# Optimization experiments

Hardware: AMD Instinct MI355X
Metric: run time of the kernel (lower is better)

Reference implementation:

```python
import jax, jax.numpy as jnp
import numpy as np

WIN = 7          # window height/width
P = 10           # prompts_len
HEADS = 12
B0 = 32          # image batch (spa_prompts batch)
NW = 64          # windows per image
NW_TOK = WIN * WIN  # 49


def _relative_position_index(w):
    coords = np.stack(np.meshgrid(np.arange(w), np.arange(w), indexing='ij'))  # [2,w,w]
    flat = coords.reshape(2, -1)                        # [2, w*w]
    rel = flat[:, :, None] - flat[:, None, :]           # [2, w*w, w*w]
    rel = rel.transpose(1, 2, 0).astype(np.int64)       # [w*w, w*w, 2]
    rel[..., 0] += w - 1
    rel[..., 1] += w - 1
    rel[..., 0] *= 2 * w - 1
    return rel.sum(-1)                                  # [w*w, w*w]

REL_IDX = jnp.asarray(_relative_position_index(WIN))    # [49,49] int


def setup_inputs() -> dict:
    key = jax.random.key(0)
    ks = jax.random.split(key, 8)
    dim = 384
    return {
        'x': jax.random.normal(ks[0], (B0 * NW, NW_TOK, dim), jnp.float32),
        'spa_prompts': jax.random.normal(ks[1], (B0, P, dim), jnp.float32),
        'mask': jax.random.normal(ks[2], (NW, NW_TOK, NW_TOK), jnp.float32),
        'bias_table': jax.random.normal(ks[3], (169, HEADS), jnp.float32) * 0.02,
        'w_qkv': jax.random.normal(ks[4], (3 * dim, dim), jnp.float32) * 0.02,
        'b_qkv': jax.random.normal(ks[5], (3 * dim,), jnp.float32) * 0.02,
        'w_proj': jax.random.normal(ks[6], (dim, dim), jnp.float32) * 0.02,
        'b_proj': jax.random.normal(ks[7], (dim,), jnp.float32) * 0.02,
    }


def reference(x, spa_prompts, mask, bias_table, w_qkv, b_qkv, w_proj, b_proj):
    B_, Nw, C = x.shape
    b0 = spa_prompts.shape[0]
    nW = B_ // b0
    hd = C // HEADS
    scale = hd ** -0.5

    # broadcast prompts to every window and prepend
    prompts = jnp.broadcast_to(spa_prompts[:, None], (b0, nW, P, C)).reshape(B_, P, C)
    xc = jnp.concatenate([prompts, x], axis=1)          # [B_, N, C], N = P + Nw
    N = xc.shape[1]

    qkv = xc @ w_qkv.T + b_qkv                          # [B_, N, 3C]
    qkv = qkv.reshape(B_, N, 3, HEADS, hd).transpose(2, 0, 3, 1, 4)
    q, k, v = qkv[0], qkv[1], qkv[2]                    # [B_, H, N, hd]

    attn_weight = jnp.einsum('bhnd,bhmd->bhnm', q, k)   # unscaled, returned

    # relative position bias gathered for the window block, padded over prompt rows/cols
    rpb = bias_table[REL_IDX.reshape(-1)].reshape(NW_TOK, NW_TOK, HEADS)
    rpb = rpb.transpose(2, 0, 1)                        # [H, 49, 49]
    bias_full = jnp.pad(rpb, ((0, 0), (P, 0), (P, 0)))  # [H, N, N]

    attn = attn_weight * scale + bias_full[None]

    mask_full = jnp.pad(mask, ((0, 0), (P, 0), (P, 0)))  # [nW, N, N]
    attn = attn.reshape(b0, nW, HEADS, N, N) + mask_full[None, :, None]
    attn = jax.nn.softmax(attn.reshape(B_, HEADS, N, N), axis=-1)

    out = jnp.einsum('bhnm,bhmd->bnhd', attn, v).reshape(B_, N, C)
    out = out @ w_proj.T + b_proj

    prompts_out = out[:, :P].reshape(b0, nW, P, C).mean(axis=1)
    x_out = out[:, P:]
    return (x_out, attn_weight, prompts_out)
```

## Files before the change

kernel.cpp:

```cpp
#include <hip/hip_runtime.h>
#include <hip/hip_bf16.h>

#define P     10
#define NTOK  59
#define HEADS 12
#define NWTOK 49

#define AW_OFF 38535168
#define PO_OFF 124096512

typedef __attribute__((ext_vector_type(8))) short short8;
typedef __attribute__((ext_vector_type(8))) unsigned short ushort8;
typedef __attribute__((ext_vector_type(4))) float floatx4;
typedef float f4u __attribute__((ext_vector_type(4), aligned(4)));
typedef unsigned int uint_g __attribute__((address_space(1)));
typedef unsigned int uint_l __attribute__((address_space(3)));

__device__ __forceinline__ unsigned short f2b(float f) {
  unsigned u = __builtin_bit_cast(unsigned, f);
  u += 0x7fffu + ((u >> 16) & 1u);
  return (unsigned short)(u >> 16);
}

__device__ __forceinline__ void gll16(const void* g, void* l) {
  __builtin_amdgcn_global_load_lds((const uint_g*)g, (uint_l*)l, 16, 0, 0);
}

__device__ __forceinline__ int xcd_swz(int bid, int nwg) {
  const int q = nwg >> 3, r = nwg & 7;
  const int xcd = bid & 7, ord = bid >> 3;
  return (xcd < r ? xcd * (q + 1) : r * (q + 1) + (xcd - r) * q) + ord;
}

__global__ __launch_bounds__(256) void convert_all_kernel(
    const float* __restrict__ x, const float* __restrict__ spa,
    const float* __restrict__ wq, const float* __restrict__ wp,
    unsigned short* __restrict__ xb, unsigned short* __restrict__ xpb,
    unsigned short* __restrict__ wqb, unsigned short* __restrict__ wpb) {
  const int bid = blockIdx.x;
  const float* src; unsigned short* dst; int base;
  if (bid < 18816)      { src = x;   dst = xb;  base = bid; }
  else if (bid < 18876) { src = spa; dst = xpb; base = bid - 18816; }
  else if (bid < 19092) { src = wq;  dst = wqb; base = bid - 18876; }
  else                  { src = wp;  dst = wpb; base = bid - 19092; }
  const int i = (base * 256 + threadIdx.x) * 8;
  const float4 a = *(const float4*)(src + i);
  const float4 b = *(const float4*)(src + i + 4);
  ushort8 o;
  o[0] = f2b(a.x); o[1] = f2b(a.y); o[2] = f2b(a.z); o[3] = f2b(a.w);
  o[4] = f2b(b.x); o[5] = f2b(b.y); o[6] = f2b(b.z); o[7] = f2b(b.w);
  *(ushort8*)(dst + i) = o;
}

__global__ __launch_bounds__(256) void combo_kernel(
    const float* __restrict__ mask, const float* __restrict__ bias_table,
    float* __restrict__ combo) {
  const int bid = blockIdx.x;
  const int h = bid % HEADS, wnd = bid / HEADS;
#pragma unroll
  for (int e0 = 0; e0 < 4096; e0 += 256) {
    const int e = e0 + threadIdx.x;
    const int ti = e >> 6, tj = e & 63;
    float v = 0.f;
    if (ti >= P && ti < NTOK && tj >= P && tj < NTOK) {
      const int a = ti - P, c = tj - P;
      const int ai = a / 7, aj = a - ai * 7;
      const int bi = c / 7, bj = c - bi * 7;
      const int ridx = (ai - bi + 6) * 13 + (aj - bj + 6);
      v = bias_table[ridx * HEADS + h] + mask[((size_t)wnd * 49 + a) * 49 + c];
    }
    combo[((size_t)bid << 12) + e] = v;
  }
}

__global__ __launch_bounds__(256) void gemm_qkv_kernel(
    const unsigned short* __restrict__ xb, const unsigned short* __restrict__ xp,
    const unsigned short* __restrict__ Bw, const float* __restrict__ b_qkv,
    unsigned short* __restrict__ qkx, unsigned short* __restrict__ qkp) {
  __shared__ unsigned short sbuf[18432];
  unsigned short* Asw = sbuf;
  unsigned short* Bsw = sbuf + 8192;
  const int t = threadIdx.x;
  const int w = t >> 6, lane = t & 63;
  const int lr = lane & 15, lg = lane >> 4;
  const int w0 = w >> 1, w1 = w & 1;
  const int wg = xcd_swz(blockIdx.x, 9 * 787);
  const int cb = wg % 9;
  const int my = wg / 9;
  const bool isP = my >= 784;
  const int n0 = cb * 128;
  const int srow = lane >> 3, cpos = lane & 7;

  floatx4 acc[4][4];
#pragma unroll
  for (int mr = 0; mr < 4; ++mr)
#pragma unroll
    for (int nc = 0; nc < 4; ++nc) acc[mr][nc] = (floatx4)0.f;

  for (int k0 = 0; k0 < 384; k0 += 64) {
#pragma unroll
    for (int i = 0; i < 4; ++i) {
      const int r = (w * 4 + i) * 8 + srow;
      const int c = cpos ^ (r & 7);
      const unsigned short* asrc;
      if (!isP) {
        asrc = xb + (size_t)(my * 128 + r) * 384 + k0 + c * 8;
      } else {
        int mp = (my - 784) * 128 + r;
        if (mp > 319) mp = 319;
        asrc = xp + (size_t)mp * 384 + k0 + c * 8;
      }
      gll16(asrc, Asw + (w * 4 + i) * 512);
      gll16(Bw + (size_t)(n0 + r) * 384 + k0 + c * 8, Bsw + (w * 4 + i) * 512);
    }
    __syncthreads();
#pragma unroll
    for (int kh = 0; kh < 2; ++kh) {
      short8 af[4], bf[4];
#pragma unroll
      for (int mr = 0; mr < 4; ++mr) {
        const int r = w0 * 64 + mr * 16 + lr;
        af[mr] = *(const short8*)(Asw + r * 64 + (((kh * 4 + lg) ^ (r & 7)) * 8));
      }
#pragma unroll
      for (int nc = 0; nc < 4; ++nc) {
        const int r = w1 * 64 + nc * 16 + lr;
        bf[nc] = *(const short8*)(Bsw + r * 64 + (((kh * 4 + lg) ^ (r & 7)) * 8));
      }
#pragma unroll
      for (int mr = 0; mr < 4; ++mr)
#pragma unroll
        for (int nc = 0; nc < 4; ++nc)
          acc[mr][nc] = __builtin_amdgcn_mfma_f32_16x16x32_bf16(
              af[mr], bf[nc], acc[mr][nc], 0, 0, 0);
    }
    __syncthreads();
  }

  const int sec = cb / 3;
  const int nis = (cb - sec * 3) * 128;
  float bias[4];
#pragma unroll
  for (int nc = 0; nc < 4; ++nc)
    bias[nc] = b_qkv[n0 + w1 * 64 + nc * 16 + lr];

  unsigned short* rp = sbuf + w * 4608;
#pragma unroll
  for (int mr = 0; mr < 4; ++mr)
#pragma unroll
    for (int nc = 0; nc < 4; ++nc)
#pragma unroll
      for (int reg = 0; reg < 4; ++reg)
        rp[(mr * 16 + lg * 4 + reg) * 72 + nc * 16 + lr] =
            f2b(acc[mr][nc][reg] + bias[nc]);
  __syncthreads();

  const int rr = lane;
  unsigned short* dst = nullptr;
  if (!isP) {
    const int m = my * 128 + w0 * 64 + rr;
    const int bb = m / 49, tok = m - bb * 49;
    dst = qkx + ((size_t)(bb * 3 + sec) * 49 + tok) * 384 + nis + w1 * 64;
  } else {
    const int mp = (my - 784) * 128 + w0 * 64 + rr;
    if (mp < 320) {
      const int b0 = mp / 10, ptok = mp - b0 * 10;
      dst = qkp + ((size_t)(b0 * 3 + sec) * 10 + ptok) * 384 + nis + w1 * 64;
    }
  }
  if (dst) {
#pragma unroll
    for (int u = 0; u < 8; ++u)
      *(ushort8*)(dst + u * 8) = *(const ushort8*)(rp + rr * 72 + u * 8);
  }
}

__global__ __launch_bounds__(256) void attn_proj_kernel(
    const unsigned short* __restrict__ qkx, const unsigned short* __restrict__ qkp,
    const float* __restrict__ combo, const unsigned short* __restrict__ wproj,
    const float* __restrict__ b_proj, float* __restrict__ aw_out,
    float* __restrict__ x_out, float* __restrict__ pbuf) {
  __shared__ char lds[74752];
  unsigned short* Obuf = (unsigned short*)lds;
  unsigned short* qs   = (unsigned short*)(lds + 50176);
  unsigned short* ks   = (unsigned short*)(lds + 55296);
  unsigned short* vt   = (unsigned short*)(lds + 60416);
  unsigned short* Bst  = (unsigned short*)(lds + 50176);

  const int b = blockIdx.x;
  const int t = threadIdx.x;
  const int w = t >> 6, lane = t & 63, lr = lane & 15, lg = lane >> 4;
  const float scale = 0.17677669529663687f;
  const int q = w * 16 + lr;

  ushort8 nq, nk, nv;
  const int srow_ = t >> 2, sdc = (t & 3) * 8;
  auto load_head = [&](int h) {
    if (t < 236) {
      if (srow_ < P) {
        const unsigned short* pb =
            qkp + ((size_t)((b >> 6) * 3) * 10 + srow_) * 384 + h * 32 + sdc;
        nq = *(const ushort8*)(pb);
        nk = *(const ushort8*)(pb + 10 * 384);
        nv = *(const ushort8*)(pb + 20 * 384);
      } else {
        const unsigned short* xbp =
            qkx + ((size_t)(b * 3) * 49 + (srow_ - P)) * 384 + h * 32 + sdc;
        nq = *(const ushort8*)(xbp);
        nk = *(const ushort8*)(xbp + 49 * 384);
        nv = *(const ushort8*)(xbp + 98 * 384);
      }
    }
  };

  if (t < 160) vt[(t / 5) * 74 + 59 + (t % 5)] = 0;
  load_head(0);

  for (int h = 0; h < HEADS; ++h) {
    __syncthreads();
    if (t < 236) {
      *(ushort8*)(qs + srow_ * 40 + sdc) = nq;
      *(ushort8*)(ks + srow_ * 40 + sdc) = nk;
#pragma unroll
      for (int j = 0; j < 8; ++j) vt[(sdc + j) * 74 + srow_] = nv[j];
    }
    __syncthreads();
    if (h + 1 < HEADS) load_head(h + 1);

    const short8 qa = *(const short8*)(qs + q * 40 + lg * 8);
    floatx4 sacc[4];
#pragma unroll
    for (int nt = 0; nt < 4; ++nt) {
      const short8 kb = *(const short8*)(ks + (nt * 16 + lr) * 40 + lg * 8);
      sacc[nt] =
          __builtin_amdgcn_mfma_f32_16x16x32_bf16(kb, qa, (floatx4)0.f, 0, 0, 0);
    }

    if (q < NTOK) {
      float* rowp = aw_out + ((size_t)(b * HEADS + h)) * 3481 + q * 59;
#pragma unroll
      for (int nt = 0; nt < 3; ++nt)
        *(f4u*)(rowp + nt * 16 + lg * 4) = __builtin_bit_cast(f4u, sacc[nt]);
      if (lg < 2) {
        *(f4u*)(rowp + 48 + lg * 4) = __builtin_bit_cast(f4u, sacc[3]);
      } else if (lg == 2) {
        rowp[56] = sacc[3][0]; rowp[57] = sacc[3][1]; rowp[58] = sacc[3][2];
      }
    }

    const float* comb =
        combo + (((size_t)((b & 63) * HEADS + h)) << 12) + q * 64;
    float ev[4][4];
    float mx = -3.0e38f;
#pragma unroll
    for (int nt = 0; nt < 4; ++nt) {
      const float4 c4 = *(const float4*)(comb + nt * 16 + lg * 4);
      const float cc[4] = {c4.x, c4.y, c4.z, c4.w};
#pragma unroll
      for (int reg = 0; reg < 4; ++reg) {
        const int kk2 = nt * 16 + lg * 4 + reg;
        const float v = (q < NTOK && kk2 < NTOK)
                            ? fmaf(sacc[nt][reg], scale, cc[reg])
                            : -3.0e38f;
        ev[nt][reg] = v;
        mx = fmaxf(mx, v);
      }
    }
    mx = fmaxf(mx, __shfl_xor(mx, 16));
    mx = fmaxf(mx, __shfl_xor(mx, 32));
    float sm = 0.f;
#pragma unroll
    for (int nt = 0; nt < 4; ++nt)
#pragma unroll
      for (int reg = 0; reg < 4; ++reg) {
        const float e = __expf(ev[nt][reg] - mx);
        ev[nt][reg] = e;
        sm += e;
      }
    sm += __shfl_xor(sm, 16);
    sm += __shfl_xor(sm, 32);
    const float inv = 1.0f / sm;

    unsigned pk[4][2];
#pragma unroll
    for (int nt = 0; nt < 4; ++nt)
#pragma unroll
      for (int pp = 0; pp < 2; ++pp)
        pk[nt][pp] = (unsigned)f2b(ev[nt][2 * pp] * inv) |
                     ((unsigned)f2b(ev[nt][2 * pp + 1] * inv) << 16);

    floatx4 oacc[2];
    oacc[0] = (floatx4)0.f; oacc[1] = (floatx4)0.f;
#pragma unroll
    for (int kk = 0; kk < 2; ++kk) {
      unsigned W4[4];
#pragma unroll
      for (int jp = 0; jp < 4; ++jp) {
        const int srcl = lr + 16 * (2 * (lg & 1) + (jp >> 1));
        const int lo = __shfl((int)pk[2 * kk][jp & 1], srcl);
        const int hi = __shfl((int)pk[2 * kk + 1][jp & 1], srcl);
        W4[jp] = (lg >> 1) ? (unsigned)hi : (unsigned)lo;
      }
      uint4 wu; wu.x = W4[0]; wu.y = W4[1]; wu.z = W4[2]; wu.w = W4[3];
      const short8 pa = __builtin_bit_cast(short8, wu);
#pragma unroll
      for (int nt = 0; nt < 2; ++nt) {
        const short8 vb =
            *(const short8*)(vt + (nt * 16 + lr) * 74 + kk * 32 + lg * 8);
        oacc[nt] =
            __builtin_amdgcn_mfma_f32_16x16x32_bf16(pa, vb, oacc[nt], 0, 0, 0);
      }
    }

#pragma unroll
    for (int nt = 0; nt < 2; ++nt)
#pragma unroll
      for (int reg = 0; reg < 4; ++reg)
        Obuf[(w * 16 + lg * 4 + reg) * 392 + h * 32 + nt * 16 + lr] =
            f2b(oacc[nt][reg]);
  }

  ushort8 bst[6];
  auto load_proj = [&](int s) {
    const int nh_ = s / 6, kch_ = s % 6;
#pragma unroll
    for (int i = 0; i < 6; ++i) {
      const int g = w * 6 + i;
      const int r = g * 8 + (lane >> 3);
      const int c = (lane & 7) ^ (r & 7);
      bst[i] = *(const ushort8*)(wproj + (size_t)(nh_ * 192 + r) * 384 +
                                 kch_ * 64 + c * 8);
    }
  };
  load_proj(0);

  floatx4 pacc[12];
#pragma unroll
  for (int nh = 0; nh < 2; ++nh) {
#pragma unroll
    for (int i = 0; i < 12; ++i) pacc[i] = (floatx4)0.f;
    for (int kch = 0; kch < 6; ++kch) {
      const int s = nh * 6 + kch;
      __syncthreads();
#pragma unroll
      for (int i = 0; i < 6; ++i)
        *(ushort8*)(Bst + (size_t)(w * 6 + i) * 512 + lane * 8) = bst[i];
      __syncthreads();
      if (s + 1 < 12) load_proj(s + 1);
#pragma unroll
      for (int kh = 0; kh < 2; ++kh) {
        const short8 af = *(const short8*)(Obuf + (w * 16 + lr) * 392 +
                                           kch * 64 + kh * 32 + lg * 8);
#pragma unroll
        for (int nc = 0; nc < 12; ++nc) {
          const int nr = nc * 16 + lr;
          const short8 bf =
              *(const short8*)(Bst + nr * 64 + (((kh * 4 + lg) ^ (nr & 7)) * 8));
          pacc[nc] =
              __builtin_amdgcn_mfma_f32_16x16x32_bf16(af, bf, pacc[nc], 0, 0, 0);
        }
      }
    }
#pragma unroll
    for (int nc = 0; nc < 12; ++nc) {
      const int n = nh * 192 + nc * 16 + lr;
      const float bias = b_proj[n];
#pragma unroll
      for (int reg = 0; reg < 4; ++reg) {
        const int row = w * 16 + lg * 4 + reg;
        if (row < NTOK) {
          float* dst = (row >= P)
              ? x_out + ((size_t)(b * NWTOK + row - P)) * 384 + n
              : pbuf + ((size_t)(b * P + row)) * 384 + n;
          *dst = pacc[nc][reg] + bias;
        }
      }
    }
  }
}

__global__ __launch_bounds__(256) void reduce_prompts_kernel(
    const float* __restrict__ pbuf, float* __restrict__ po) {
  const int o = blockIdx.x * 256 + threadIdx.x;
  const int b0 = o / 3840;
  const int rem = o - b0 * 3840;
  const float* base = pbuf + (size_t)b0 * 64 * 3840 + rem;
  float s = 0.f;
#pragma unroll 8
  for (int w = 0; w < 64; ++w) s += base[(size_t)w * 3840];
  po[o] = s * (1.f / 64.f);
}

extern "C" void kernel_launch(void* const* d_in, const int* in_sizes, int n_in,
                              void* d_out, int out_size, void* d_ws, size_t ws_size,
                              hipStream_t stream) {
  const float* x          = (const float*)d_in[0];
  const float* spa        = (const float*)d_in[1];
  const float* mask       = (const float*)d_in[2];
  const float* bias_table = (const float*)d_in[3];
  const float* w_qkv      = (const float*)d_in[4];
  const float* b_qkv      = (const float*)d_in[5];
  const float* w_proj     = (const float*)d_in[6];
  const float* b_proj     = (const float*)d_in[7];
  float* out = (float*)d_out;

  unsigned short* x_bf     = (unsigned short*)d_ws;
  unsigned short* xp_bf    = (unsigned short*)((char*)d_ws + 77070336ULL);
  unsigned short* wqkv_bf  = (unsigned short*)((char*)d_ws + 77316096ULL);
  unsigned short* qkx      = (unsigned short*)((char*)d_ws + 92798976ULL);
  unsigned short* qkp      = (unsigned short*)((char*)d_ws + 324009984ULL);
  unsigned short* wproj_bf = (unsigned short*)((char*)d_ws + 324747264ULL);
  float*          pbuf     = (float*)((char*)d_ws + 325042176ULL);
  float*          combo    = (float*)((char*)d_ws + 356499456ULL);

  convert_all_kernel<<<19164, 256, 0, stream>>>(x, spa, w_qkv, w_proj,
                                                x_bf, xp_bf, wqkv_bf, wproj_bf);
  combo_kernel<<<768, 256, 0, stream>>>(mask, bias_table, combo);
  gemm_qkv_kernel<<<9 * 787, 256, 0, stream>>>(x_bf, xp_bf, wqkv_bf, b_qkv,
                                               qkx, qkp);
  attn_proj_kernel<<<2048, 256, 0, stream>>>(qkx, qkp, combo, wproj_bf, b_proj,
                                             out + AW_OFF, out, pbuf);
  reduce_prompts_kernel<<<480, 256, 0, stream>>>(pbuf, out + PO_OFF);
}
```

Baseline: 587.6 us.

## Double attention block to 512 threads, processing two heads concurrently

```diff
diff --git a/kernel.cpp b/kernel.cpp
--- a/kernel.cpp
+++ b/kernel.cpp
@@ -175,28 +175,37 @@
   }
 }
 
-__global__ __launch_bounds__(256) void attn_proj_kernel(
+__global__ __launch_bounds__(512, 4) void attn_proj_kernel(
     const unsigned short* __restrict__ qkx, const unsigned short* __restrict__ qkp,
     const float* __restrict__ combo, const unsigned short* __restrict__ wproj,
     const float* __restrict__ b_proj, float* __restrict__ aw_out,
     float* __restrict__ x_out, float* __restrict__ pbuf) {
-  __shared__ char lds[74752];
+  __shared__ char lds[80128];
   unsigned short* Obuf = (unsigned short*)lds;
-  unsigned short* qs   = (unsigned short*)(lds + 50176);
-  unsigned short* ks   = (unsigned short*)(lds + 55296);
-  unsigned short* vt   = (unsigned short*)(lds + 60416);
-  unsigned short* Bst  = (unsigned short*)(lds + 50176);
+  unsigned short* Bst = (unsigned short*)(lds + 50176);
 
   const int b = blockIdx.x;
   const int t = threadIdx.x;
   const int w = t >> 6, lane = t & 63, lr = lane & 15, lg = lane >> 4;
+  const int hgrp = w >> 2;
+  const int wq = w & 3;
   const float scale = 0.17677669529663687f;
-  const int q = w * 16 + lr;
+  const int q = wq * 16 + lr;
+
+  unsigned short* qs = (unsigned short*)(lds + 50176 + hgrp * 14976);
+  unsigned short* ks = (unsigned short*)(lds + 50176 + hgrp * 14976 + 5120);
+  unsigned short* vt = (unsigned short*)(lds + 50176 + hgrp * 14976 + 10240);
+
+  const int tt = t & 255, sgrp = t >> 8;
+  const int srow_ = tt >> 2, sdc = (tt & 3) * 8;
+  unsigned short* qsS = (unsigned short*)(lds + 50176 + sgrp * 14976);
+  unsigned short* ksS = qsS + 2560;
+  unsigned short* vtS = qsS + 5120;
 
   ushort8 nq, nk, nv;
-  const int srow_ = t >> 2, sdc = (t & 3) * 8;
-  auto load_head = [&](int h) {
-    if (t < 236) {
+  auto load_head = [&](int rpair) {
+    if (tt < 236) {
+      const int h = rpair * 2 + sgrp;
       if (srow_ < P) {
         const unsigned short* pb =
             qkp + ((size_t)((b >> 6) * 3) * 10 + srow_) * 384 + h * 32 + sdc;
@@ -213,19 +222,24 @@
     }
   };
 
-  if (t < 160) vt[(t / 5) * 74 + 59 + (t % 5)] = 0;
+  if (t < 320) {
+    const int g2 = t / 160, e = t - g2 * 160;
+    unsigned short* vtZ = (unsigned short*)(lds + 50176 + g2 * 14976 + 10240);
+    vtZ[(e / 5) * 74 + 59 + (e % 5)] = 0;
+  }
   load_head(0);
 
-  for (int h = 0; h < HEADS; ++h) {
+  for (int r = 0; r < 6; ++r) {
+    const int h = r * 2 + hgrp;
     __syncthreads();
-    if (t < 236) {
-      *(ushort8*)(qs + srow_ * 40 + sdc) = nq;
-      *(ushort8*)(ks + srow_ * 40 + sdc) = nk;
-#pragma unroll
-      for (int j = 0; j < 8; ++j) vt[(sdc + j) * 74 + srow_] = nv[j];
+    if (tt < 236) {
+      *(ushort8*)(qsS + srow_ * 40 + sdc) = nq;
+      *(ushort8*)(ksS + srow_ * 40 + sdc) = nk;
+#pragma unroll
+      for (int j = 0; j < 8; ++j) vtS[(sdc + j) * 74 + srow_] = nv[j];
     }
     __syncthreads();
-    if (h + 1 < HEADS) load_head(h + 1);
+    if (r + 1 < 6) load_head(r + 1);
 
     const short8 qa = *(const short8*)(qs + q * 40 + lg * 8);
     floatx4 sacc[4];
@@ -316,16 +330,17 @@
     for (int nt = 0; nt < 2; ++nt)
 #pragma unroll
       for (int reg = 0; reg < 4; ++reg)
-        Obuf[(w * 16 + lg * 4 + reg) * 392 + h * 32 + nt * 16 + lr] =
+        Obuf[(wq * 16 + lg * 4 + reg) * 392 + h * 32 + nt * 16 + lr] =
             f2b(oacc[nt][reg]);
   }
 
-  ushort8 bst[6];
+  const int rw = w & 3, ng = w >> 2;
+  ushort8 bst[3];
   auto load_proj = [&](int s) {
     const int nh_ = s / 6, kch_ = s % 6;
 #pragma unroll
-    for (int i = 0; i < 6; ++i) {
-      const int g = w * 6 + i;
+    for (int i = 0; i < 3; ++i) {
+      const int g = w * 3 + i;
       const int r = g * 8 + (lane >> 3);
       const int c = (lane & 7) ^ (r & 7);
       bst[i] = *(const ushort8*)(wproj + (size_t)(nh_ * 192 + r) * 384 +
@@ -334,26 +349,26 @@
   };
   load_proj(0);
 
-  floatx4 pacc[12];
+  floatx4 pacc[6];
 #pragma unroll
   for (int nh = 0; nh < 2; ++nh) {
 #pragma unroll
-    for (int i = 0; i < 12; ++i) pacc[i] = (floatx4)0.f;
+    for (int i = 0; i < 6; ++i) pacc[i] = (floatx4)0.f;
     for (int kch = 0; kch < 6; ++kch) {
       const int s = nh * 6 + kch;
       __syncthreads();
 #pragma unroll
-      for (int i = 0; i < 6; ++i)
-        *(ushort8*)(Bst + (size_t)(w * 6 + i) * 512 + lane * 8) = bst[i];
+      for (int i = 0; i < 3; ++i)
+        *(ushort8*)(Bst + (size_t)(w * 3 + i) * 512 + lane * 8) = bst[i];
       __syncthreads();
       if (s + 1 < 12) load_proj(s + 1);
 #pragma unroll
       for (int kh = 0; kh < 2; ++kh) {
-        const short8 af = *(const short8*)(Obuf + (w * 16 + lr) * 392 +
+        const short8 af = *(const short8*)(Obuf + (rw * 16 + lr) * 392 +
                                            kch * 64 + kh * 32 + lg * 8);
 #pragma unroll
-        for (int nc = 0; nc < 12; ++nc) {
-          const int nr = nc * 16 + lr;
+        for (int nc = 0; nc < 6; ++nc) {
+          const int nr = ng * 96 + nc * 16 + lr;
           const short8 bf =
               *(const short8*)(Bst + nr * 64 + (((kh * 4 + lg) ^ (nr & 7)) * 8));
           pacc[nc] =
@@ -362,12 +377,12 @@
       }
     }
 #pragma unroll
-    for (int nc = 0; nc < 12; ++nc) {
-      const int n = nh * 192 + nc * 16 + lr;
+    for (int nc = 0; nc < 6; ++nc) {
+      const int n = nh * 192 + ng * 96 + nc * 16 + lr;
       const float bias = b_proj[n];
 #pragma unroll
       for (int reg = 0; reg < 4; ++reg) {
-        const int row = w * 16 + lg * 4 + reg;
+        const int row = rw * 16 + lg * 4 + reg;
         if (row < NTOK) {
           float* dst = (row >= P)
               ? x_out + ((size_t)(b * NWTOK + row - P)) * 384 + n
@@ -418,7 +433,7 @@
   combo_kernel<<<768, 256, 0, stream>>>(mask, bias_table, combo);
   gemm_qkv_kernel<<<9 * 787, 256, 0, stream>>>(x_bf, xp_bf, wqkv_bf, b_qkv,
                                                qkx, qkp);
-  attn_proj_kernel<<<2048, 256, 0, stream>>>(qkx, qkp, combo, wproj_bf, b_proj,
+  attn_proj_kernel<<<2048, 512, 0, stream>>>(qkx, qkp, combo, wproj_bf, b_proj,
                                              out + AW_OFF, out, pbuf);
   reduce_prompts_kernel<<<480, 256, 0, stream>>>(pbuf, out + PO_OFF);
 }
```

After: 542.3 us. 1.08x faster.
